# Performance work log

Hardware: AMD Instinct MI355X
Metric: run time of the kernel (lower is better)

The kernel has to match this reference:

```python
import jax, jax.numpy as jnp
import numpy as np

N_NODES = 50000
N_EDGES = 800000
IN_DIM = 128
HEADS = 8
F_OUT = 16


def setup_inputs() -> dict:
    key = jax.random.key(0)
    ks = jax.random.split(key, 7)
    x = jax.random.normal(ks[0], (N_NODES, IN_DIM), dtype=jnp.float32)
    edge_index = jax.random.randint(ks[1], (2, N_EDGES), 0, N_NODES, dtype=jnp.int32)
    # xavier-normal-ish scale
    W_proj = jax.random.normal(ks[2], (HEADS * F_OUT, IN_DIM), dtype=jnp.float32) * (2.0 / (IN_DIM + HEADS * F_OUT)) ** 0.5
    a_src = jax.random.normal(ks[3], (HEADS, F_OUT), dtype=jnp.float32) * 0.1
    a_tgt = jax.random.normal(ks[4], (HEADS, F_OUT), dtype=jnp.float32) * 0.1
    W_skip = jax.random.normal(ks[5], (HEADS * F_OUT, IN_DIM), dtype=jnp.float32) * (2.0 / (IN_DIM + HEADS * F_OUT)) ** 0.5
    bias = jnp.zeros((HEADS * F_OUT,), dtype=jnp.float32)
    return {"x": x, "edge_index": edge_index, "W_proj": W_proj, "a_src": a_src,
            "a_tgt": a_tgt, "W_skip": W_skip, "bias": bias}


def reference(x, edge_index, W_proj, a_src, a_tgt, W_skip, bias):
    N = x.shape[0]
    src, tgt = edge_index[0], edge_index[1]
    # project: [N, H, F]
    proj = (x @ W_proj.T).reshape(N, HEADS, F_OUT)
    # per-node partial scores: [N, H]
    s_src = jnp.einsum('nhf,hf->nh', proj, a_src)
    s_tgt = jnp.einsum('nhf,hf->nh', proj, a_tgt)
    # per-edge scores, LeakyReLU(0.2): [E, H]
    e = jax.nn.leaky_relu(s_src[src] + s_tgt[tgt], negative_slope=0.2)
    # segment softmax over incoming edges of each target node
    e_max = jax.ops.segment_max(e, tgt, num_segments=N)
    e_exp = jnp.exp(e - e_max[tgt])
    denom = jax.ops.segment_sum(e_exp, tgt, num_segments=N)
    alpha = e_exp / (denom[tgt] + 1e-16)  # [E, H]
    # weighted scatter-add of projected source features: [N, H, F]
    msgs = proj[src] * alpha[:, :, None]
    out = jax.ops.segment_sum(msgs, tgt, num_segments=N)
    # skip connection (in_dim != out_dim path -> skip_proj), concat heads, bias, ELU
    out = out + (x @ W_skip.T).reshape(N, HEADS, F_OUT)
    out = out.reshape(N, HEADS * F_OUT) + bias
    return jax.nn.elu(out)
```

## Files before the change

kernel.cpp:

```cpp
#include <hip/hip_runtime.h>
#include <hip/hip_bf16.h>
#include <math.h>

#define PADN 50048
#define CAP 64

typedef __attribute__((ext_vector_type(8))) short short8;
typedef __attribute__((ext_vector_type(4))) float f32x4;

__device__ __forceinline__ unsigned short f2b(float f) {
  __hip_bfloat16 h = __float2bfloat16(f);
  return *(unsigned short*)&h;
}

__global__ __launch_bounds__(256) void k_prep(const float* __restrict__ Wp,
                                              const float* __restrict__ Ws,
                                              const float* __restrict__ a_src,
                                              const float* __restrict__ a_tgt,
                                              const int* __restrict__ ei,
                                              unsigned short* __restrict__ Bpk,
                                              int* __restrict__ counts,
                                              int* __restrict__ rank,
                                              int E, int cntB) {
  const int b = blockIdx.x;
  if (b < cntB) {
    const int tid = b * 256 + threadIdx.x;
    const int T = cntB * 256;
    const int* tgtp = ei + E;
    int e[4], t[4], r[4];
#pragma unroll
    for (int p = 0; p < 4; ++p) {
      e[p] = tid + p * T;
      t[p] = (e[p] < E) ? tgtp[e[p]] : 0;
    }
#pragma unroll
    for (int p = 0; p < 4; ++p)
      r[p] = (e[p] < E) ? atomicAdd(&counts[t[p]], 1) : 0;
#pragma unroll
    for (int p = 0; p < 4; ++p)
      if (e[p] < E) rank[e[p]] = r[p];
    return;
  }
  int idx = (b - cntB) * 256 + threadIdx.x;
  int tile = idx >> 8;
  int ks = (idx >> 6) & 3;
  int lane = idx & 63;
  int kbase = ks * 32 + (lane >> 4) * 8;
  unsigned short o[8];
  if (tile < 16) {
    int col = tile * 16 + (lane & 15);
    const float* src = (col < 128) ? (Wp + (size_t)col * 128 + kbase)
                                   : (Ws + (size_t)(col - 128) * 128 + kbase);
#pragma unroll
    for (int j = 0; j < 8; ++j) o[j] = f2b(src[j]);
  } else {
    int col = lane & 15;
    int h = col & 7;
    const float* av = (col < 8) ? (a_src + h * 16) : (a_tgt + h * 16);
#pragma unroll
    for (int j = 0; j < 8; ++j) {
      int k = kbase + j;
      float s = 0.f;
#pragma unroll
      for (int f = 0; f < 16; ++f) s = fmaf(Wp[(size_t)(h * 16 + f) * 128 + k], av[f], s);
      o[j] = f2b(s);
    }
  }
  *(short8*)(Bpk + (size_t)idx * 8) = *(short8*)o;
}

__global__ __launch_bounds__(256) void k_gemm_place(
    const float* __restrict__ x, const unsigned short* __restrict__ Bpk,
    unsigned short* __restrict__ pb, unsigned short* __restrict__ sb,
    float* __restrict__ ssrc, float* __restrict__ stgt,
    const int* __restrict__ ei, const int* __restrict__ rank,
    int* __restrict__ esrc, int N, int E, int placeB) {
  const int b = blockIdx.x;
  if (b < placeB) {
    const int tid = b * 256 + threadIdx.x;
    const int T = placeB * 256;
    const int* srcp = ei;
    const int* tgtp = ei + E;
#pragma unroll
    for (int p = 0; p < 8; ++p) {
      int e = tid + p * T;
      if (e < E) {
        int r = rank[e];
        if (r < CAP) esrc[(tgtp[e] << 6) + r] = srcp[e];
      }
    }
    return;
  }

  const int wave = threadIdx.x >> 6, lane = threadIdx.x & 63;
  const int m = lane & 15, q = lane >> 4;
  const int r0 = (b - placeB) * 64 + wave * 16;
  const int row_a = r0 + m;

  short8 a[4];
#pragma unroll
  for (int ks = 0; ks < 4; ++ks) {
    float4 v0 = make_float4(0.f, 0.f, 0.f, 0.f), v1 = v0;
    if (row_a < N) {
      const float4* xp = (const float4*)(x + (size_t)row_a * 128 + ks * 32 + q * 8);
      v0 = xp[0];
      v1 = xp[1];
    }
    unsigned short o[8];
    o[0] = f2b(v0.x); o[1] = f2b(v0.y); o[2] = f2b(v0.z); o[3] = f2b(v0.w);
    o[4] = f2b(v1.x); o[5] = f2b(v1.y); o[6] = f2b(v1.z); o[7] = f2b(v1.w);
    a[ks] = *(short8*)o;
  }

  for (int ct = 0; ct < 16; ++ct) {
    f32x4 acc = {0.f, 0.f, 0.f, 0.f};
#pragma unroll
    for (int ks = 0; ks < 4; ++ks) {
      short8 bfr = *(const short8*)(Bpk + (size_t)((ct * 4 + ks) * 64 + lane) * 8);
      acc = __builtin_amdgcn_mfma_f32_16x16x32_bf16(a[ks], bfr, acc, 0, 0, 0);
    }
    unsigned short* dst = (ct < 8) ? pb : sb;
    const int cc = (ct & 7) * 16 + m;
#pragma unroll
    for (int r = 0; r < 4; ++r) {
      int row = r0 + q * 4 + r;
      if (row < N) dst[(size_t)row * 128 + cc] = f2b(acc[r]);
    }
  }
  {
    f32x4 acc = {0.f, 0.f, 0.f, 0.f};
#pragma unroll
    for (int ks = 0; ks < 4; ++ks) {
      short8 bfr = *(const short8*)(Bpk + (size_t)((16 * 4 + ks) * 64 + lane) * 8);
      acc = __builtin_amdgcn_mfma_f32_16x16x32_bf16(a[ks], bfr, acc, 0, 0, 0);
    }
    float* sd = (m < 8) ? ssrc : stgt;
    const int h = m & 7;
#pragma unroll
    for (int r = 0; r < 4; ++r) {
      int row = r0 + q * 4 + r;
      if (row < N) sd[row * 8 + h] = acc[r];
    }
  }
}

__global__ __launch_bounds__(256) void k_agg(const unsigned short* __restrict__ pb,
                                             const unsigned short* __restrict__ sb,
                                             const float* __restrict__ ssrc,
                                             const float* __restrict__ stgt,
                                             const float* __restrict__ bias,
                                             const int* __restrict__ counts,
                                             const int* __restrict__ esrc,
                                             float* __restrict__ out, int N) {
  int wid = (int)((blockIdx.x * (size_t)blockDim.x + threadIdx.x) >> 6);
  int lane = threadIdx.x & 63;
  if (wid >= N) return;
  const int n = wid;
  const int c = lane * 2;
  const int h = lane >> 3;

  const float st = stgt[n * 8 + h];
  const int cnt = min(counts[n], CAP);

  float ds0 = 0.f, ds1 = 0.f, ds2 = 0.f, ds3 = 0.f;
  float x00 = 0.f, x01 = 0.f, x10 = 0.f, x11 = 0.f;
  float x20 = 0.f, x21 = 0.f, x30 = 0.f, x31 = 0.f;

#define FILLQ(p, jj)                                              \
  {                                                               \
    int s_ = __builtin_amdgcn_readlane(srcv, (jj));               \
    pv##p = *(const unsigned int*)(pb + (size_t)s_ * 128 + c);    \
    sc##p = ssrc[s_ * 8 + h];                                     \
  }
#define EDGEQ(p, dsx, a0x, a1x)                                   \
  {                                                               \
    float e_ = sc##p + st;                                        \
    e_ = fmaxf(e_, 0.2f * e_);                                    \
    float w_ = __expf(e_);                                        \
    dsx += w_;                                                    \
    a0x = fmaf(w_, __uint_as_float(pv##p << 16), a0x);            \
    a1x = fmaf(w_, __uint_as_float(pv##p & 0xffff0000u), a1x);    \
  }

  if (cnt > 0) {
    const int cm = cnt - 1;
    int srcv = esrc[(n << 6) + min(lane, cm)];
    unsigned int pv0, pv1, pv2, pv3, pv4, pv5, pv6, pv7;
    float sc0, sc1, sc2, sc3, sc4, sc5, sc6, sc7;

    FILLQ(0, 0)
    FILLQ(1, min(1, cm))
    FILLQ(2, min(2, cm))
    FILLQ(3, min(3, cm))
    FILLQ(4, min(4, cm))
    FILLQ(5, min(5, cm))
    FILLQ(6, min(6, cm))
    FILLQ(7, min(7, cm))

    int j = 0;
    for (; j + 8 <= cnt; j += 8) {
      EDGEQ(0, ds0, x00, x01)
      EDGEQ(1, ds1, x10, x11)
      EDGEQ(2, ds2, x20, x21)
      EDGEQ(3, ds3, x30, x31)
      if (j + 8 < cnt) {
        FILLQ(0, min(j + 8, cm))
        FILLQ(1, min(j + 9, cm))
        FILLQ(2, min(j + 10, cm))
        FILLQ(3, min(j + 11, cm))
      }
      EDGEQ(4, ds0, x00, x01)
      EDGEQ(5, ds1, x10, x11)
      EDGEQ(6, ds2, x20, x21)
      EDGEQ(7, ds3, x30, x31)
      if (j + 12 < cnt) {
        FILLQ(4, min(j + 12, cm))
        FILLQ(5, min(j + 13, cm))
        FILLQ(6, min(j + 14, cm))
        FILLQ(7, min(j + 15, cm))
      }
    }
    const int rem = cnt - j;
    if (rem > 0) EDGEQ(0, ds0, x00, x01)
    if (rem > 1) EDGEQ(1, ds1, x10, x11)
    if (rem > 2) EDGEQ(2, ds2, x20, x21)
    if (rem > 3) EDGEQ(3, ds3, x30, x31)
    if (rem > 4) EDGEQ(4, ds0, x00, x01)
    if (rem > 5) EDGEQ(5, ds1, x10, x11)
    if (rem > 6) EDGEQ(6, ds2, x20, x21)
  }
#undef FILLQ
#undef EDGEQ

  const float dsum = (ds0 + ds1) + (ds2 + ds3);
  const float acc0 = (x00 + x10) + (x20 + x30);
  const float acc1 = (x01 + x11) + (x21 + x31);
  const float inv = 1.0f / (dsum + 1e-16f);
  size_t row = (size_t)n * 128;
  unsigned int su = *(const unsigned int*)(sb + row + c);
  float sk0 = __uint_as_float(su << 16);
  float sk1 = __uint_as_float(su & 0xffff0000u);
  float r0 = fmaf(acc0, inv, sk0) + bias[c];
  float r1 = fmaf(acc1, inv, sk1) + bias[c + 1];
  r0 = (r0 > 0.f) ? r0 : (__expf(r0) - 1.0f);
  r1 = (r1 > 0.f) ? r1 : (__expf(r1) - 1.0f);
  *(float2*)(out + row + c) = make_float2(r0, r1);
}

extern "C" void kernel_launch(void* const* d_in, const int* in_sizes, int n_in,
                              void* d_out, int out_size, void* d_ws, size_t ws_size,
                              hipStream_t stream) {
  const float* x = (const float*)d_in[0];
  const int* ei = (const int*)d_in[1];
  const float* Wp = (const float*)d_in[2];
  const float* a_src = (const float*)d_in[3];
  const float* a_tgt = (const float*)d_in[4];
  const float* Ws = (const float*)d_in[5];
  const float* bias = (const float*)d_in[6];
  float* out = (float*)d_out;

  const int N = in_sizes[0] / 128;
  const int E = in_sizes[1] / 2;

  unsigned short* Bpk = (unsigned short*)d_ws;
  unsigned short* pb = Bpk + 34816;
  unsigned short* sb = pb + (size_t)N * 128;
  float* ssrc = (float*)(sb + (size_t)N * 128);
  float* stgt = ssrc + (size_t)N * 8;
  int* counts = (int*)(stgt + (size_t)N * 8);
  int* rank = counts + N;
  int* esrc = rank + E;

  const int cntB = (E + 4 * 256 - 1) / (4 * 256);
  const int placeB = (E + 8 * 256 - 1) / (8 * 256);
  const int gemmB = PADN / 64;

  hipMemsetAsync(counts, 0, (size_t)N * sizeof(int), stream);
  k_prep<<<cntB + 17, 256, 0, stream>>>(Wp, Ws, a_src, a_tgt, ei, Bpk, counts,
                                        rank, E, cntB);
  k_gemm_place<<<placeB + gemmB, 256, 0, stream>>>(x, Bpk, pb, sb, ssrc, stgt,
                                                   ei, rank, esrc, N, E, placeB);
  k_agg<<<(N + 3) / 4, 256, 0, stream>>>(pb, sb, ssrc, stgt, bias, counts, esrc, out, N);
}
```

Measured before the change: 190.8 us.

## Overlap edge counting with GEMM and fold counter zeroing into init kernel

Moves the per-target atomic edge counting out of the prep kernel and into the GEMM kernel, so the atomics run alongside the projection MFMA blocks. The hipMemsetAsync of the counters is replaced by zeroing blocks inside the init kernel. Edge placement becomes its own kernel launched after the GEMM. The aim is to hide the atomic counting latency behind GEMM work and drop the memset call, at the cost of one extra kernel launch.

```diff
diff --git a/kernel.cpp b/kernel.cpp
--- a/kernel.cpp
+++ b/kernel.cpp
@@ -13,35 +13,20 @@
   return *(unsigned short*)&h;
 }
 
-__global__ __launch_bounds__(256) void k_prep(const float* __restrict__ Wp,
+__global__ __launch_bounds__(256) void k_init(const float* __restrict__ Wp,
                                               const float* __restrict__ Ws,
                                               const float* __restrict__ a_src,
                                               const float* __restrict__ a_tgt,
-                                              const int* __restrict__ ei,
                                               unsigned short* __restrict__ Bpk,
                                               int* __restrict__ counts,
-                                              int* __restrict__ rank,
-                                              int E, int cntB) {
+                                              int N, int zeroB) {
   const int b = blockIdx.x;
-  if (b < cntB) {
-    const int tid = b * 256 + threadIdx.x;
-    const int T = cntB * 256;
-    const int* tgtp = ei + E;
-    int e[4], t[4], r[4];
-#pragma unroll
-    for (int p = 0; p < 4; ++p) {
-      e[p] = tid + p * T;
-      t[p] = (e[p] < E) ? tgtp[e[p]] : 0;
-    }
-#pragma unroll
-    for (int p = 0; p < 4; ++p)
-      r[p] = (e[p] < E) ? atomicAdd(&counts[t[p]], 1) : 0;
-#pragma unroll
-    for (int p = 0; p < 4; ++p)
-      if (e[p] < E) rank[e[p]] = r[p];
+  if (b < zeroB) {
+    int i = b * 256 + threadIdx.x;
+    if (i < N) counts[i] = 0;
     return;
   }
-  int idx = (b - cntB) * 256 + threadIdx.x;
+  int idx = (b - zeroB) * 256 + threadIdx.x;
   int tile = idx >> 8;
   int ks = (idx >> 6) & 3;
   int lane = idx & 63;
@@ -69,32 +54,35 @@
   *(short8*)(Bpk + (size_t)idx * 8) = *(short8*)o;
 }
 
-__global__ __launch_bounds__(256) void k_gemm_place(
+__global__ __launch_bounds__(256) void k_cg(
     const float* __restrict__ x, const unsigned short* __restrict__ Bpk,
     unsigned short* __restrict__ pb, unsigned short* __restrict__ sb,
     float* __restrict__ ssrc, float* __restrict__ stgt,
-    const int* __restrict__ ei, const int* __restrict__ rank,
-    int* __restrict__ esrc, int N, int E, int placeB) {
+    const int* __restrict__ ei, int* __restrict__ counts,
+    int* __restrict__ rank, int N, int E, int cntB) {
   const int b = blockIdx.x;
-  if (b < placeB) {
+  if (b < cntB) {
     const int tid = b * 256 + threadIdx.x;
-    const int T = placeB * 256;
-    const int* srcp = ei;
+    const int T = cntB * 256;
     const int* tgtp = ei + E;
+    int e[8], t[8], r[8];
 #pragma unroll
     for (int p = 0; p < 8; ++p) {
-      int e = tid + p * T;
-      if (e < E) {
-        int r = rank[e];
-        if (r < CAP) esrc[(tgtp[e] << 6) + r] = srcp[e];
-      }
-    }
+      e[p] = tid + p * T;
+      t[p] = (e[p] < E) ? tgtp[e[p]] : 0;
+    }
+#pragma unroll
+    for (int p = 0; p < 8; ++p)
+      r[p] = (e[p] < E) ? atomicAdd(&counts[t[p]], 1) : 0;
+#pragma unroll
+    for (int p = 0; p < 8; ++p)
+      if (e[p] < E) rank[e[p]] = r[p];
     return;
   }
 
   const int wave = threadIdx.x >> 6, lane = threadIdx.x & 63;
   const int m = lane & 15, q = lane >> 4;
-  const int r0 = (b - placeB) * 64 + wave * 16;
+  const int r0 = (b - cntB) * 64 + wave * 16;
   const int row_a = r0 + m;
 
   short8 a[4];
@@ -140,6 +128,23 @@
     for (int r = 0; r < 4; ++r) {
       int row = r0 + q * 4 + r;
       if (row < N) sd[row * 8 + h] = acc[r];
+    }
+  }
+}
+
+__global__ __launch_bounds__(256) void k_place(const int* __restrict__ ei,
+                                               const int* __restrict__ rank,
+                                               int* __restrict__ esrc, int E) {
+  const int tid = blockIdx.x * 256 + threadIdx.x;
+  const int T = gridDim.x * 256;
+  const int* srcp = ei;
+  const int* tgtp = ei + E;
+#pragma unroll
+  for (int p = 0; p < 8; ++p) {
+    int e = tid + p * T;
+    if (e < E) {
+      int r = rank[e];
+      if (r < CAP) esrc[(tgtp[e] << 6) + r] = srcp[e];
     }
   }
 }
@@ -271,14 +276,14 @@
   int* rank = counts + N;
   int* esrc = rank + E;
 
-  const int cntB = (E + 4 * 256 - 1) / (4 * 256);
-  const int placeB = (E + 8 * 256 - 1) / (8 * 256);
+  const int zeroB = (N + 255) / 256;
+  const int cntB = (E + 8 * 256 - 1) / (8 * 256);
   const int gemmB = PADN / 64;
-
-  hipMemsetAsync(counts, 0, (size_t)N * sizeof(int), stream);
-  k_prep<<<cntB + 17, 256, 0, stream>>>(Wp, Ws, a_src, a_tgt, ei, Bpk, counts,
-                                        rank, E, cntB);
-  k_gemm_place<<<placeB + gemmB, 256, 0, stream>>>(x, Bpk, pb, sb, ssrc, stgt,
-                                                   ei, rank, esrc, N, E, placeB);
+  const int placeB = cntB;
+
+  k_init<<<zeroB + 17, 256, 0, stream>>>(Wp, Ws, a_src, a_tgt, Bpk, counts, N, zeroB);
+  k_cg<<<cntB + gemmB, 256, 0, stream>>>(x, Bpk, pb, sb, ssrc, stgt, ei, counts,
+                                         rank, N, E, cntB);
+  k_place<<<placeB, 256, 0, stream>>>(ei, rank, esrc, E);
   k_agg<<<(N + 3) / 4, 256, 0, stream>>>(pb, sb, ssrc, stgt, bias, counts, esrc, out, N);
 }
```

Result: no change. 189.7 us (-0.6%).

## Build per-target edge buckets with block-partitioned LDS atomics instead of global atomics

Applied to the files above, without the earlier changes.

Replaces the global-atomic counting pass, the rank array and the separate placement pass with one build kernel. Each of 256 blocks owns a contiguous range of target nodes, scans all edge targets, and uses shared-memory atomics to bucket the edges it owns. This removes the memset, the global atomics and the rank round-trip, and splits the GEMM into its own kernel. The trade is that every block reads the whole target array (256x redundant reads, mostly served from L2), and bucket order within a node is now nondeterministic.

```diff
diff --git a/kernel.cpp b/kernel.cpp
--- a/kernel.cpp
+++ b/kernel.cpp
@@ -4,6 +4,7 @@
 
 #define PADN 50048
 #define CAP 64
+#define NBLD 256
 
 typedef __attribute__((ext_vector_type(8))) short short8;
 typedef __attribute__((ext_vector_type(4))) float f32x4;
@@ -13,88 +14,100 @@
   return *(unsigned short*)&h;
 }
 
-__global__ __launch_bounds__(256) void k_prep(const float* __restrict__ Wp,
-                                              const float* __restrict__ Ws,
-                                              const float* __restrict__ a_src,
-                                              const float* __restrict__ a_tgt,
-                                              const int* __restrict__ ei,
-                                              unsigned short* __restrict__ Bpk,
-                                              int* __restrict__ counts,
-                                              int* __restrict__ rank,
-                                              int E, int cntB) {
+__global__ __launch_bounds__(256) void k_build(const float* __restrict__ Wp,
+                                               const float* __restrict__ Ws,
+                                               const float* __restrict__ a_src,
+                                               const float* __restrict__ a_tgt,
+                                               const int* __restrict__ ei,
+                                               unsigned short* __restrict__ Bpk,
+                                               int* __restrict__ counts,
+                                               int* __restrict__ esrc,
+                                               int E, int N) {
   const int b = blockIdx.x;
-  if (b < cntB) {
-    const int tid = b * 256 + threadIdx.x;
-    const int T = cntB * 256;
-    const int* tgtp = ei + E;
-    int e[4], t[4], r[4];
-#pragma unroll
-    for (int p = 0; p < 4; ++p) {
-      e[p] = tid + p * T;
-      t[p] = (e[p] < E) ? tgtp[e[p]] : 0;
-    }
-#pragma unroll
-    for (int p = 0; p < 4; ++p)
-      r[p] = (e[p] < E) ? atomicAdd(&counts[t[p]], 1) : 0;
-#pragma unroll
-    for (int p = 0; p < 4; ++p)
-      if (e[p] < E) rank[e[p]] = r[p];
+  if (b >= NBLD) {
+    int idx = (b - NBLD) * 256 + threadIdx.x;
+    int tile = idx >> 8;
+    int ks = (idx >> 6) & 3;
+    int lane = idx & 63;
+    int kbase = ks * 32 + (lane >> 4) * 8;
+    unsigned short o[8];
+    if (tile < 16) {
+      int col = tile * 16 + (lane & 15);
+      const float* src = (col < 128) ? (Wp + (size_t)col * 128 + kbase)
+                                     : (Ws + (size_t)(col - 128) * 128 + kbase);
+#pragma unroll
+      for (int j = 0; j < 8; ++j) o[j] = f2b(src[j]);
+    } else {
+      int col = lane & 15;
+      int h = col & 7;
+      const float* av = (col < 8) ? (a_src + h * 16) : (a_tgt + h * 16);
+#pragma unroll
+      for (int j = 0; j < 8; ++j) {
+        int k = kbase + j;
+        float s = 0.f;
+#pragma unroll
+        for (int f = 0; f < 16; ++f)
+          s = fmaf(Wp[(size_t)(h * 16 + f) * 128 + k], av[f], s);
+        o[j] = f2b(s);
+      }
+    }
+    *(short8*)(Bpk + (size_t)idx * 8) = *(short8*)o;
     return;
   }
-  int idx = (b - cntB) * 256 + threadIdx.x;
-  int tile = idx >> 8;
-  int ks = (idx >> 6) & 3;
-  int lane = idx & 63;
-  int kbase = ks * 32 + (lane >> 4) * 8;
-  unsigned short o[8];
-  if (tile < 16) {
-    int col = tile * 16 + (lane & 15);
-    const float* src = (col < 128) ? (Wp + (size_t)col * 128 + kbase)
-                                   : (Ws + (size_t)(col - 128) * 128 + kbase);
-#pragma unroll
-    for (int j = 0; j < 8; ++j) o[j] = f2b(src[j]);
-  } else {
-    int col = lane & 15;
-    int h = col & 7;
-    const float* av = (col < 8) ? (a_src + h * 16) : (a_tgt + h * 16);
-#pragma unroll
-    for (int j = 0; j < 8; ++j) {
-      int k = kbase + j;
-      float s = 0.f;
-#pragma unroll
-      for (int f = 0; f < 16; ++f) s = fmaf(Wp[(size_t)(h * 16 + f) * 128 + k], av[f], s);
-      o[j] = f2b(s);
-    }
-  }
-  *(short8*)(Bpk + (size_t)idx * 8) = *(short8*)o;
-}
-
-__global__ __launch_bounds__(256) void k_gemm_place(
+
+  __shared__ int lc[256];
+  const int span = (N + NBLD - 1) / NBLD;
+  const int lo = b * span;
+  const int sp = (lo < N) ? min(span, N - lo) : 0;
+  lc[threadIdx.x] = 0;
+  __syncthreads();
+
+  const int* srcp = ei;
+  const int4* tg4 = (const int4*)(ei + E);
+  const int nt4 = E >> 2;
+
+#define PROC1(t, e)                                                        \
+  {                                                                        \
+    unsigned d_ = (unsigned)((t) - lo);                                    \
+    if (d_ < (unsigned)sp) {                                               \
+      int r_ = atomicAdd(&lc[d_], 1);                                      \
+      if (r_ < CAP) esrc[((size_t)(lo + (int)d_) << 6) + r_] = srcp[e];    \
+    }                                                                      \
+  }
+#define PROC4(v, e0)                                                       \
+  PROC1((v).x, (e0)) PROC1((v).y, (e0) + 1) PROC1((v).z, (e0) + 2)         \
+  PROC1((v).w, (e0) + 3)
+
+  int i = threadIdx.x;
+  for (; i + 768 < nt4; i += 1024) {
+    int4 A = tg4[i];
+    int4 B = tg4[i + 256];
+    int4 C = tg4[i + 512];
+    int4 D = tg4[i + 768];
+    PROC4(A, i << 2)
+    PROC4(B, (i + 256) << 2)
+    PROC4(C, (i + 512) << 2)
+    PROC4(D, (i + 768) << 2)
+  }
+  for (; i < nt4; i += 256) {
+    int4 A = tg4[i];
+    PROC4(A, i << 2)
+  }
+  for (int e = (nt4 << 2) + threadIdx.x; e < E; e += 256) PROC1(ei[E + e], e)
+#undef PROC1
+#undef PROC4
+
+  __syncthreads();
+  for (int k = threadIdx.x; k < sp; k += 256) counts[lo + k] = lc[k];
+}
+
+__global__ __launch_bounds__(256) void k_gemm(
     const float* __restrict__ x, const unsigned short* __restrict__ Bpk,
     unsigned short* __restrict__ pb, unsigned short* __restrict__ sb,
-    float* __restrict__ ssrc, float* __restrict__ stgt,
-    const int* __restrict__ ei, const int* __restrict__ rank,
-    int* __restrict__ esrc, int N, int E, int placeB) {
-  const int b = blockIdx.x;
-  if (b < placeB) {
-    const int tid = b * 256 + threadIdx.x;
-    const int T = placeB * 256;
-    const int* srcp = ei;
-    const int* tgtp = ei + E;
-#pragma unroll
-    for (int p = 0; p < 8; ++p) {
-      int e = tid + p * T;
-      if (e < E) {
-        int r = rank[e];
-        if (r < CAP) esrc[(tgtp[e] << 6) + r] = srcp[e];
-      }
-    }
-    return;
-  }
-
+    float* __restrict__ ssrc, float* __restrict__ stgt, int N) {
   const int wave = threadIdx.x >> 6, lane = threadIdx.x & 63;
   const int m = lane & 15, q = lane >> 4;
-  const int r0 = (b - placeB) * 64 + wave * 16;
+  const int r0 = blockIdx.x * 64 + wave * 16;
   const int row_a = r0 + m;
 
   short8 a[4];
@@ -268,17 +281,10 @@
   float* ssrc = (float*)(sb + (size_t)N * 128);
   float* stgt = ssrc + (size_t)N * 8;
   int* counts = (int*)(stgt + (size_t)N * 8);
-  int* rank = counts + N;
-  int* esrc = rank + E;
-
-  const int cntB = (E + 4 * 256 - 1) / (4 * 256);
-  const int placeB = (E + 8 * 256 - 1) / (8 * 256);
-  const int gemmB = PADN / 64;
-
-  hipMemsetAsync(counts, 0, (size_t)N * sizeof(int), stream);
-  k_prep<<<cntB + 17, 256, 0, stream>>>(Wp, Ws, a_src, a_tgt, ei, Bpk, counts,
-                                        rank, E, cntB);
-  k_gemm_place<<<placeB + gemmB, 256, 0, stream>>>(x, Bpk, pb, sb, ssrc, stgt,
-                                                   ei, rank, esrc, N, E, placeB);
+  int* esrc = counts + N;
+
+  k_build<<<NBLD + 17, 256, 0, stream>>>(Wp, Ws, a_src, a_tgt, ei, Bpk, counts,
+                                         esrc, E, N);
+  k_gemm<<<PADN / 64, 256, 0, stream>>>(x, Bpk, pb, sb, ssrc, stgt, N);
   k_agg<<<(N + 3) / 4, 256, 0, stream>>>(pb, sb, ssrc, stgt, bias, counts, esrc, out, N);
 }
```

Result: slower. 401.6 us (+110.5%).
